# Kernel optimization log

Measured on AMD Instinct MI355X. Metric: run time of the kernel, lower is better.

The kernel has to match this reference:

```python
import jax, jax.numpy as jnp
import numpy as np

D = 64          # feature dim
H_POS = 64      # pos_mlp hidden
H_ATTN = 4 * D  # attn_mlp hidden
B, N = 1, 1024


def setup_inputs() -> dict:
    key = jax.random.key(0)
    ks = jax.random.split(key, 12)
    s = lambda fan_in: 1.0 / np.sqrt(fan_in)
    return {
        "x": jax.random.normal(ks[0], (B, N, D), jnp.float32),
        "pos": jax.random.normal(ks[1], (B, N, 2), jnp.float32),
        "Wq": jax.random.normal(ks[2], (D, D), jnp.float32) * s(D),
        "Wk": jax.random.normal(ks[3], (D, D), jnp.float32) * s(D),
        "Wv": jax.random.normal(ks[4], (D, D), jnp.float32) * s(D),
        "pW1": jax.random.normal(ks[5], (2, H_POS), jnp.float32) * s(2),
        "pb1": jnp.zeros((H_POS,), jnp.float32),
        "pW2": jax.random.normal(ks[6], (H_POS, D), jnp.float32) * s(H_POS),
        "pb2": jnp.zeros((D,), jnp.float32),
        "aW1": jax.random.normal(ks[7], (D, H_ATTN), jnp.float32) * s(D),
        "ab1": jnp.zeros((H_ATTN,), jnp.float32),
        "aW2": jax.random.normal(ks[8], (H_ATTN, D), jnp.float32) * s(H_ATTN),
        "ab2": jnp.zeros((D,), jnp.float32),
    }


def reference(x, pos, Wq, Wk, Wv, pW1, pb1, pW2, pb2, aW1, ab1, aW2, ab2):
    # projections: [b, n, d]
    q = x @ Wq
    k = x @ Wk
    v = x @ Wv
    # pairwise relative positions: [b, i, j, 2]
    rel_pos = pos[:, :, None, :] - pos[:, None, :, :]
    # pos MLP: [b, i, j, d]
    rpe = jax.nn.relu(rel_pos @ pW1 + pb1) @ pW2 + pb2
    # pairwise q - k: [b, i, j, d]
    qk_rel = q[:, :, None, :] - k[:, None, :, :]
    # values broadcast over i, plus positional embedding: [b, i, j, d]
    vv = v[:, None, :, :] + rpe
    # attention MLP on (qk_rel + rpe): [b, i, j, d]
    sim = jax.nn.relu((qk_rel + rpe) @ aW1 + ab1) @ aW2 + ab2
    # softmax over j (axis=-2), per-channel
    attn = jax.nn.softmax(sim, axis=-2)
    # weighted aggregation: [b, i, d]
    agg = jnp.einsum('bijd,bijd->bid', attn, vv)
    return agg
```

## Files before the change

### kernel.cpp

```cpp
#include <hip/hip_runtime.h>


typedef float f32x4 __attribute__((ext_vector_type(4)));
typedef int   i32x8 __attribute__((ext_vector_type(8)));
using sh8 = __attribute__((ext_vector_type(8))) short;

static constexpr int NPTS = 1024;

#if __has_builtin(__builtin_amdgcn_exp2f)
#define EXP2(x) __builtin_amdgcn_exp2f(x)
#else
#define EXP2(x) exp2f(x)
#endif

static constexpr size_t BEXT_OFF = 0;
static constexpr size_t AW2F_OFF = 65536;
static constexpr size_t PW2F_OFF = 98304;
static constexpr size_t CARR_OFF = 106496;
static constexpr size_t AI_OFF   = 107520;
static constexpr size_t QI_OFF   = 369664;
static constexpr size_t VPT_OFF  = 631808;
static constexpr size_t AJ_OFF   = 893952;
static constexpr size_t KN_OFF   = 1025024;

__device__ __forceinline__ unsigned short f2b_rne(float f) {
    unsigned u = __float_as_uint(f);
    u += 0x7fffu + ((u >> 16) & 1u);
    return (unsigned short)(u >> 16);
}
__device__ __forceinline__ unsigned pk2(float lo, float hi) {
    return __builtin_amdgcn_perm(__float_as_uint(hi), __float_as_uint(lo), 0x07060302);
}
__device__ __forceinline__ float b2f(unsigned short s) {
    return __uint_as_float(((unsigned)s) << 16);
}
__device__ __forceinline__ unsigned char f2fp8(float v) {
    return (unsigned char)(__builtin_amdgcn_cvt_pk_fp8_f32(v, 0.f, 0, false) & 0xff);
}
__device__ __forceinline__ unsigned pk4fp8(float a, float b, float c, float d) {
    int r = __builtin_amdgcn_cvt_pk_fp8_f32(a, b, 0, false);
    r = __builtin_amdgcn_cvt_pk_fp8_f32(c, d, r, true);
    return (unsigned)r;
}
__device__ __forceinline__ i32x8 ld32B(const void* p) {
    const uint4 a = ((const uint4*)p)[0];
    const uint4 b = ((const uint4*)p)[1];
    i32x8 r;
    r[0] = a.x; r[1] = a.y; r[2] = a.z; r[3] = a.w;
    r[4] = b.x; r[5] = b.y; r[6] = b.z; r[7] = b.w;
    return r;
}

__global__ void prep_all(const float* __restrict__ x, const float* __restrict__ pos,
                         const float* __restrict__ Wq, const float* __restrict__ Wk,
                         const float* __restrict__ Wv, const float* __restrict__ pW1,
                         const float* __restrict__ pb1, const float* __restrict__ pW2,
                         const float* __restrict__ pb2, const float* __restrict__ aW1,
                         const float* __restrict__ ab1, const float* __restrict__ aW2,
                         unsigned short* __restrict__ bextf, unsigned char* __restrict__ aw2f8,
                         unsigned short* __restrict__ pw2f, float* __restrict__ cArr,
                         float* __restrict__ qI, unsigned short* __restrict__ kN,
                         float* __restrict__ vPT, float* __restrict__ aI,
                         unsigned short* __restrict__ aJ)
{
    const int b = blockIdx.x;
    if (b < 209) {
        const int idx = b * 256 + threadIdx.x;
        if (idx < 32768) {
            const int k = idx >> 8, t = idx & 255;
            float val;
            if (k < 64) {
                float s = 0.f;
                for (int d = 0; d < 64; ++d) s = fmaf(pW2[k * 64 + d], aW1[d * 256 + t], s);
                val = s;
            } else {
                val = aW1[(k - 64) * 256 + t];
            }
            const int kc = k >> 5, kl = k & 31, qq = kl >> 3, e = kl & 7;
            const int ntg = t >> 4, tl = t & 15;
            bextf[(((size_t)(kc * 16 + ntg) * 64) + (qq * 16 + tl)) * 8 + e] = f2b_rne(val);
        } else if (idx < 49152) {
            const int r = idx - 32768;
            const int e = r & 31, lane = (r >> 5) & 63, wsl = (r >> 11) & 3, kb = r >> 13;
            const int q = lane >> 4, dl = lane & 15;
            const int kp = kb * 128 + q * 32 + e;
            const int t = 64 * (kp >> 6) + 16 * (kp & 3) + ((kp >> 2) & 15);
            const int d = 16 * wsl + dl;
            aw2f8[r] = f2fp8(aW2[t * 64 + d] * 1.4426950408889634f);
        } else if (idx < 53248) {
            const int r = idx - 49152;
            const int k = r >> 6, d = r & 63;
            const int kc = k >> 5, kl = k & 31, qq = kl >> 3, e = kl & 7;
            const int nt = d >> 4, dl = d & 15;
            pw2f[(((size_t)(kc * 4 + nt) * 64) + (qq * 16 + dl)) * 8 + e] = f2b_rne(pW2[k * 64 + d]);
        } else if (idx < 53504) {
            const int t = idx - 53248;
            float s = ab1[t];
            for (int d = 0; d < 64; ++d) s = fmaf(pb2[d], aW1[d * 256 + t], s);
            cArr[t] = s;
        }
    } else {
        const int t = threadIdx.x, sub = t >> 6, d = t & 63;
        const int i = (b - 209) * 4 + sub;
        __shared__ float xs[4][64];
        xs[sub][d] = x[i * 64 + d];
        __syncthreads();
        float q = 0.f, k = 0.f, v = 0.f;
        for (int e = 0; e < 64; ++e) {
            const float xe = xs[sub][e];
            q = fmaf(xe, Wq[e * 64 + d], q);
            k = fmaf(xe, Wk[e * 64 + d], k);
            v = fmaf(xe, Wv[e * 64 + d], v);
        }
        const float a = pos[i * 2] * pW1[d] + pos[i * 2 + 1] * pW1[64 + d];
        qI[i * 64 + d] = q;
        kN[i * 64 + d] = f2b_rne(-k);
        vPT[d * NPTS + i] = v + pb2[d];
        aI[i * 64 + d] = a + pb1[d];
        aJ[i * 64 + d] = f2b_rne(a);
    }
}

__global__ __launch_bounds__(256, 2) void ptl_main(
    const float* __restrict__ aI, const float* __restrict__ qI,
    const unsigned short* __restrict__ aJ, const unsigned short* __restrict__ kN,
    const float* __restrict__ vPT,
    const unsigned short* __restrict__ bextf, const unsigned char* __restrict__ aw2f8,
    const unsigned short* __restrict__ pw2f, const float* __restrict__ cArr,
    float* __restrict__ out)
{
    const int i    = blockIdx.x;
    const int tid  = threadIdx.x;
    const int w    = tid >> 6;
    const int lane = tid & 63;
    const int m    = lane & 15;
    const int q    = lane >> 4;

    __shared__ __align__(16) uint4 AfL[2][2][4][64];
    __shared__ __align__(16) unsigned char Hs[2][2][16 * 272];

    sh8 Bf[16];
#pragma unroll
    for (int kc = 0; kc < 4; ++kc)
#pragma unroll
        for (int nt = 0; nt < 4; ++nt)
            Bf[kc * 4 + nt] = *(const sh8*)(bextf + ((size_t)((kc * 16 + 4 * w + nt) * 64 + lane)) * 8);
    i32x8 W2f[2];
#pragma unroll
    for (int kb = 0; kb < 2; ++kb)
        W2f[kb] = ld32B(aw2f8 + ((size_t)((kb * 4 + w) * 64 + lane)) * 32);
    sh8 P2f[2];
#pragma unroll
    for (int kc = 0; kc < 2; ++kc)
        P2f[kc] = *(const sh8*)(pw2f + ((size_t)((kc * 4 + w) * 64 + lane)) * 8);

    float creg[4];
#pragma unroll
    for (int nt = 0; nt < 4; ++nt) creg[nt] = cArr[64 * w + 16 * nt + m];

    const int  half   = w & 1;
    const bool isRelu = (w < 2);
    const unsigned short* bsrc  = (isRelu ? aJ : kN) + m * 64 + half * 32 + q * 8;
    const float*          ibase = (isRelu ? aI : qI) + i * 64 + half * 32 + q * 8;
    float iv[8];
    *(float4*)(iv)     = *(const float4*)(ibase);
    *(float4*)(iv + 4) = *(const float4*)(ibase + 4);

#pragma unroll
    for (int s = 0; s < 2; ++s) {
        const sh8 raw = *(const sh8*)(bsrc + (size_t)(16 * s) * 64);
        float t[8];
#pragma unroll
        for (int e = 0; e < 8; ++e)
            t[e] = isRelu ? fmaxf(iv[e] - b2f((unsigned short)raw[e]), 0.f)
                          : iv[e] + b2f((unsigned short)raw[e]);
        uint4 pk;
        pk.x = pk2(t[0], t[1]); pk.y = pk2(t[2], t[3]);
        pk.z = pk2(t[4], t[5]); pk.w = pk2(t[6], t[7]);
        AfL[0][s][w][lane] = pk;
    }
    __syncthreads();

    float num = 0.f, den = 0.f;
    const f32x4 z4 = {0.f, 0.f, 0.f, 0.f};
    const float* vbase = vPT + (size_t)(16 * w + m) * NPTS;

    for (int n = 0; n < 32; ++n) {
        const int pb = n & 1, nb = pb ^ 1;
        const int j0 = n << 5;

        sh8 raw0, raw1;
        if (n < 31) {
            raw0 = *(const sh8*)(bsrc + (size_t)(j0 + 32) * 64);
            raw1 = *(const sh8*)(bsrc + (size_t)(j0 + 48) * 64);
        }
        const float4 vj0 = *(const float4*)(vbase + j0 + 4 * q);
        const float4 vj1 = *(const float4*)(vbase + j0 + 16 + 4 * q);

        const sh8 A00 = *(const sh8*)&AfL[pb][0][0][lane];
        const sh8 A01 = *(const sh8*)&AfL[pb][0][1][lane];
        const sh8 A02 = *(const sh8*)&AfL[pb][0][2][lane];
        const sh8 A03 = *(const sh8*)&AfL[pb][0][3][lane];
        {
            f32x4 acc[4];
#pragma unroll
            for (int nt = 0; nt < 4; ++nt) {
                const f32x4 cv = {creg[nt], creg[nt], creg[nt], creg[nt]};
                acc[nt] = __builtin_amdgcn_mfma_f32_16x16x32_bf16(A00, Bf[0 * 4 + nt], cv, 0, 0, 0);
                acc[nt] = __builtin_amdgcn_mfma_f32_16x16x32_bf16(A01, Bf[1 * 4 + nt], acc[nt], 0, 0, 0);
                acc[nt] = __builtin_amdgcn_mfma_f32_16x16x32_bf16(A02, Bf[2 * 4 + nt], acc[nt], 0, 0, 0);
                acc[nt] = __builtin_amdgcn_mfma_f32_16x16x32_bf16(A03, Bf[3 * 4 + nt], acc[nt], 0, 0, 0);
            }
            unsigned char* hw = Hs[pb][0] + (4 * q) * 272 + 64 * w + 4 * m;
#pragma unroll
            for (int r = 0; r < 4; ++r)
                *(unsigned*)(hw + r * 272) = pk4fp8(fmaxf(acc[0][r], 0.f), fmaxf(acc[1][r], 0.f),
                                                   fmaxf(acc[2][r], 0.f), fmaxf(acc[3][r], 0.f));
        }

        const sh8 A10 = *(const sh8*)&AfL[pb][1][0][lane];
        const sh8 A11 = *(const sh8*)&AfL[pb][1][1][lane];
        const sh8 A12 = *(const sh8*)&AfL[pb][1][2][lane];
        const sh8 A13 = *(const sh8*)&AfL[pb][1][3][lane];
        {
            f32x4 acc[4];
#pragma unroll
            for (int nt = 0; nt < 4; ++nt) {
                const f32x4 cv = {creg[nt], creg[nt], creg[nt], creg[nt]};
                acc[nt] = __builtin_amdgcn_mfma_f32_16x16x32_bf16(A10, Bf[0 * 4 + nt], cv, 0, 0, 0);
                acc[nt] = __builtin_amdgcn_mfma_f32_16x16x32_bf16(A11, Bf[1 * 4 + nt], acc[nt], 0, 0, 0);
                acc[nt] = __builtin_amdgcn_mfma_f32_16x16x32_bf16(A12, Bf[2 * 4 + nt], acc[nt], 0, 0, 0);
                acc[nt] = __builtin_amdgcn_mfma_f32_16x16x32_bf16(A13, Bf[3 * 4 + nt], acc[nt], 0, 0, 0);
            }
            unsigned char* hw = Hs[pb][1] + (4 * q) * 272 + 64 * w + 4 * m;
#pragma unroll
            for (int r = 0; r < 4; ++r)
                *(unsigned*)(hw + r * 272) = pk4fp8(fmaxf(acc[0][r], 0.f), fmaxf(acc[1][r], 0.f),
                                                   fmaxf(acc[2][r], 0.f), fmaxf(acc[3][r], 0.f));
        }

        const f32x4 vc0 = {vj0.x, vj0.y, vj0.z, vj0.w};
        const f32x4 vc1 = {vj1.x, vj1.y, vj1.z, vj1.w};
        f32x4 aR0 = __builtin_amdgcn_mfma_f32_16x16x32_bf16(A00, P2f[0], vc0, 0, 0, 0);
        aR0 = __builtin_amdgcn_mfma_f32_16x16x32_bf16(A01, P2f[1], aR0, 0, 0, 0);
        f32x4 aR1 = __builtin_amdgcn_mfma_f32_16x16x32_bf16(A10, P2f[0], vc1, 0, 0, 0);
        aR1 = __builtin_amdgcn_mfma_f32_16x16x32_bf16(A11, P2f[1], aR1, 0, 0, 0);

        if (n < 31) {
#pragma unroll
            for (int s = 0; s < 2; ++s) {
                const sh8 raw = s ? raw1 : raw0;
                float t[8];
#pragma unroll
                for (int e = 0; e < 8; ++e)
                    t[e] = isRelu ? fmaxf(iv[e] - b2f((unsigned short)raw[e]), 0.f)
                                  : iv[e] + b2f((unsigned short)raw[e]);
                uint4 pk;
                pk.x = pk2(t[0], t[1]); pk.y = pk2(t[2], t[3]);
                pk.z = pk2(t[4], t[5]); pk.w = pk2(t[6], t[7]);
                AfL[nb][s][w][lane] = pk;
            }
        }

        __syncthreads();

        f32x4 aS0 = z4, aS1 = z4;
#pragma unroll
        for (int kb = 0; kb < 2; ++kb) {
            const i32x8 h0 = ld32B(Hs[pb][0] + m * 272 + kb * 128 + 32 * q);
            aS0 = __builtin_amdgcn_mfma_scale_f32_16x16x128_f8f6f4(
                h0, W2f[kb], aS0, 0, 0, 0, 127, 0, 127);
            const i32x8 h1 = ld32B(Hs[pb][1] + m * 272 + kb * 128 + 32 * q);
            aS1 = __builtin_amdgcn_mfma_scale_f32_16x16x128_f8f6f4(
                h1, W2f[kb], aS1, 0, 0, 0, 127, 0, 127);
        }

#pragma unroll
        for (int r = 0; r < 4; ++r) {
            const float e0 = EXP2(aS0[r]);
            num = fmaf(e0, aR0[r], num);
            den += e0;
            const float e1 = EXP2(aS1[r]);
            num = fmaf(e1, aR1[r], num);
            den += e1;
        }
    }

    num += __shfl_xor(num, 16);
    num += __shfl_xor(num, 32);
    den += __shfl_xor(den, 16);
    den += __shfl_xor(den, 32);
    if (q == 0) out[i * 64 + 16 * w + m] = num / den;
}

extern "C" void kernel_launch(void* const* d_in, const int* in_sizes, int n_in,
                              void* d_out, int out_size, void* d_ws, size_t ws_size,
                              hipStream_t stream) {
    const float* x   = (const float*)d_in[0];
    const float* pos = (const float*)d_in[1];
    const float* Wq  = (const float*)d_in[2];
    const float* Wk  = (const float*)d_in[3];
    const float* Wv  = (const float*)d_in[4];
    const float* pW1 = (const float*)d_in[5];
    const float* pb1 = (const float*)d_in[6];
    const float* pW2 = (const float*)d_in[7];
    const float* pb2 = (const float*)d_in[8];
    const float* aW1 = (const float*)d_in[9];
    const float* ab1 = (const float*)d_in[10];
    const float* aW2 = (const float*)d_in[11];

    char* ws = (char*)d_ws;
    unsigned short* bextf = (unsigned short*)(ws + BEXT_OFF);
    unsigned char*  aw2f8 = (unsigned char*)(ws + AW2F_OFF);
    unsigned short* pw2f  = (unsigned short*)(ws + PW2F_OFF);
    float*          cArr  = (float*)(ws + CARR_OFF);
    float*          aIa   = (float*)(ws + AI_OFF);
    float*          qIa   = (float*)(ws + QI_OFF);
    float*          vPTa  = (float*)(ws + VPT_OFF);
    unsigned short* aJa   = (unsigned short*)(ws + AJ_OFF);
    unsigned short* kNa   = (unsigned short*)(ws + KN_OFF);

    prep_all<<<465, 256, 0, stream>>>(x, pos, Wq, Wk, Wv, pW1, pb1, pW2, pb2, aW1, ab1, aW2,
                                      bextf, aw2f8, pw2f, cArr, qIa, kNa, vPTa, aIa, aJa);
    ptl_main<<<NPTS, 256, 0, stream>>>(aIa, qIa, aJa, kNa, vPTa, bextf, aw2f8, pw2f, cArr,
                                       (float*)d_out);
}
```

Baseline: 183.2 us.

## Software-pipeline second-layer MLP and softmax accumulation by one iteration

```diff
diff --git a/kernel.cpp b/kernel.cpp
--- a/kernel.cpp
+++ b/kernel.cpp
@@ -183,6 +183,7 @@
 
     float num = 0.f, den = 0.f;
     const f32x4 z4 = {0.f, 0.f, 0.f, 0.f};
+    f32x4 aRp0 = z4, aRp1 = z4;
     const float* vbase = vPT + (size_t)(16 * w + m) * NPTS;
 
     for (int n = 0; n < 32; ++n) {
@@ -218,6 +219,14 @@
                                                    fmaxf(acc[2][r], 0.f), fmaxf(acc[3][r], 0.f));
         }
 
+        i32x8 h00, h01, h10, h11;
+        if (n) {
+            h00 = ld32B(Hs[nb][0] + m * 272 + 0   + 32 * q);
+            h01 = ld32B(Hs[nb][0] + m * 272 + 128 + 32 * q);
+            h10 = ld32B(Hs[nb][1] + m * 272 + 0   + 32 * q);
+            h11 = ld32B(Hs[nb][1] + m * 272 + 128 + 32 * q);
+        }
+
         const sh8 A10 = *(const sh8*)&AfL[pb][1][0][lane];
         const sh8 A11 = *(const sh8*)&AfL[pb][1][1][lane];
         const sh8 A12 = *(const sh8*)&AfL[pb][1][2][lane];
@@ -239,12 +248,35 @@
                                                    fmaxf(acc[2][r], 0.f), fmaxf(acc[3][r], 0.f));
         }
 
+        if (n) {
+            f32x4 aS0 = z4, aS1 = z4;
+            aS0 = __builtin_amdgcn_mfma_scale_f32_16x16x128_f8f6f4(
+                h00, W2f[0], aS0, 0, 0, 0, 127, 0, 127);
+            aS0 = __builtin_amdgcn_mfma_scale_f32_16x16x128_f8f6f4(
+                h01, W2f[1], aS0, 0, 0, 0, 127, 0, 127);
+            aS1 = __builtin_amdgcn_mfma_scale_f32_16x16x128_f8f6f4(
+                h10, W2f[0], aS1, 0, 0, 0, 127, 0, 127);
+            aS1 = __builtin_amdgcn_mfma_scale_f32_16x16x128_f8f6f4(
+                h11, W2f[1], aS1, 0, 0, 0, 127, 0, 127);
+#pragma unroll
+            for (int r = 0; r < 4; ++r) {
+                const float e0 = EXP2(aS0[r]);
+                num = fmaf(e0, aRp0[r], num);
+                den += e0;
+                const float e1 = EXP2(aS1[r]);
+                num = fmaf(e1, aRp1[r], num);
+                den += e1;
+            }
+        }
+
         const f32x4 vc0 = {vj0.x, vj0.y, vj0.z, vj0.w};
         const f32x4 vc1 = {vj1.x, vj1.y, vj1.z, vj1.w};
         f32x4 aR0 = __builtin_amdgcn_mfma_f32_16x16x32_bf16(A00, P2f[0], vc0, 0, 0, 0);
         aR0 = __builtin_amdgcn_mfma_f32_16x16x32_bf16(A01, P2f[1], aR0, 0, 0, 0);
         f32x4 aR1 = __builtin_amdgcn_mfma_f32_16x16x32_bf16(A10, P2f[0], vc1, 0, 0, 0);
         aR1 = __builtin_amdgcn_mfma_f32_16x16x32_bf16(A11, P2f[1], aR1, 0, 0, 0);
+        aRp0 = aR0;
+        aRp1 = aR1;
 
         if (n < 31) {
 #pragma unroll
@@ -263,25 +295,29 @@
         }
 
         __syncthreads();
-
+    }
+
+    {
         f32x4 aS0 = z4, aS1 = z4;
-#pragma unroll
-        for (int kb = 0; kb < 2; ++kb) {
-            const i32x8 h0 = ld32B(Hs[pb][0] + m * 272 + kb * 128 + 32 * q);
-            aS0 = __builtin_amdgcn_mfma_scale_f32_16x16x128_f8f6f4(
-                h0, W2f[kb], aS0, 0, 0, 0, 127, 0, 127);
-            const i32x8 h1 = ld32B(Hs[pb][1] + m * 272 + kb * 128 + 32 * q);
-            aS1 = __builtin_amdgcn_mfma_scale_f32_16x16x128_f8f6f4(
-                h1, W2f[kb], aS1, 0, 0, 0, 127, 0, 127);
-        }
-
+        const i32x8 h00 = ld32B(Hs[1][0] + m * 272 + 0   + 32 * q);
+        const i32x8 h01 = ld32B(Hs[1][0] + m * 272 + 128 + 32 * q);
+        const i32x8 h10 = ld32B(Hs[1][1] + m * 272 + 0   + 32 * q);
+        const i32x8 h11 = ld32B(Hs[1][1] + m * 272 + 128 + 32 * q);
+        aS0 = __builtin_amdgcn_mfma_scale_f32_16x16x128_f8f6f4(
+            h00, W2f[0], aS0, 0, 0, 0, 127, 0, 127);
+        aS0 = __builtin_amdgcn_mfma_scale_f32_16x16x128_f8f6f4(
+            h01, W2f[1], aS0, 0, 0, 0, 127, 0, 127);
+        aS1 = __builtin_amdgcn_mfma_scale_f32_16x16x128_f8f6f4(
+            h10, W2f[0], aS1, 0, 0, 0, 127, 0, 127);
+        aS1 = __builtin_amdgcn_mfma_scale_f32_16x16x128_f8f6f4(
+            h11, W2f[1], aS1, 0, 0, 0, 127, 0, 127);
 #pragma unroll
         for (int r = 0; r < 4; ++r) {
             const float e0 = EXP2(aS0[r]);
-            num = fmaf(e0, aR0[r], num);
+            num = fmaf(e0, aRp0[r], num);
             den += e0;
             const float e1 = EXP2(aS1[r]);
-            num = fmaf(e1, aR1[r], num);
+            num = fmaf(e1, aRp1[r], num);
             den += e1;
         }
     }
```

Result: no change. 180.8 us (-1.3%).

## Process two query points per block and software-pipeline the second attention GEMM

Applied to the files above, without the earlier changes.

```diff
diff --git a/kernel.cpp b/kernel.cpp
--- a/kernel.cpp
+++ b/kernel.cpp
@@ -129,15 +129,15 @@
     const unsigned short* __restrict__ pw2f, const float* __restrict__ cArr,
     float* __restrict__ out)
 {
-    const int i    = blockIdx.x;
+    const int i0   = blockIdx.x * 2;
     const int tid  = threadIdx.x;
     const int w    = tid >> 6;
     const int lane = tid & 63;
     const int m    = lane & 15;
     const int q    = lane >> 4;
 
-    __shared__ __align__(16) uint4 AfL[2][2][4][64];
-    __shared__ __align__(16) unsigned char Hs[2][2][16 * 272];
+    __shared__ __align__(16) uint4 AfL[2][2][2][4][64];
+    __shared__ __align__(16) unsigned char Hs[2][2][2][16 * 272];
 
     sh8 Bf[16];
 #pragma unroll
@@ -160,47 +160,38 @@
 
     const int  half   = w & 1;
     const bool isRelu = (w < 2);
-    const unsigned short* bsrc  = (isRelu ? aJ : kN) + m * 64 + half * 32 + q * 8;
-    const float*          ibase = (isRelu ? aI : qI) + i * 64 + half * 32 + q * 8;
-    float iv[8];
-    *(float4*)(iv)     = *(const float4*)(ibase);
-    *(float4*)(iv + 4) = *(const float4*)(ibase + 4);
-
-#pragma unroll
-    for (int s = 0; s < 2; ++s) {
-        const sh8 raw = *(const sh8*)(bsrc + (size_t)(16 * s) * 64);
-        float t[8];
-#pragma unroll
-        for (int e = 0; e < 8; ++e)
-            t[e] = isRelu ? fmaxf(iv[e] - b2f((unsigned short)raw[e]), 0.f)
-                          : iv[e] + b2f((unsigned short)raw[e]);
-        uint4 pk;
-        pk.x = pk2(t[0], t[1]); pk.y = pk2(t[2], t[3]);
-        pk.z = pk2(t[4], t[5]); pk.w = pk2(t[6], t[7]);
-        AfL[0][s][w][lane] = pk;
-    }
-    __syncthreads();
-
-    float num = 0.f, den = 0.f;
-    const f32x4 z4 = {0.f, 0.f, 0.f, 0.f};
-    const float* vbase = vPT + (size_t)(16 * w + m) * NPTS;
-
-    for (int n = 0; n < 32; ++n) {
-        const int pb = n & 1, nb = pb ^ 1;
-        const int j0 = n << 5;
-
-        sh8 raw0, raw1;
-        if (n < 31) {
-            raw0 = *(const sh8*)(bsrc + (size_t)(j0 + 32) * 64);
-            raw1 = *(const sh8*)(bsrc + (size_t)(j0 + 48) * 64);
-        }
-        const float4 vj0 = *(const float4*)(vbase + j0 + 4 * q);
-        const float4 vj1 = *(const float4*)(vbase + j0 + 16 + 4 * q);
-
-        const sh8 A00 = *(const sh8*)&AfL[pb][0][0][lane];
-        const sh8 A01 = *(const sh8*)&AfL[pb][0][1][lane];
-        const sh8 A02 = *(const sh8*)&AfL[pb][0][2][lane];
-        const sh8 A03 = *(const sh8*)&AfL[pb][0][3][lane];
+    const unsigned short* bsrc = (isRelu ? aJ : kN) + m * 64 + half * 32 + q * 8;
+    const float* ib0 = (isRelu ? aI : qI) + (size_t)i0 * 64 + half * 32 + q * 8;
+    const float* ib1 = ib0 + 64;
+    float iv0[8], iv1[8];
+    *(float4*)(iv0)     = *(const float4*)(ib0);
+    *(float4*)(iv0 + 4) = *(const float4*)(ib0 + 4);
+    *(float4*)(iv1)     = *(const float4*)(ib1);
+    *(float4*)(iv1 + 4) = *(const float4*)(ib1 + 4);
+
+    auto build2 = [&](int buf, int s, const sh8& raw) {
+        float t0[8], t1[8];
+#pragma unroll
+        for (int e = 0; e < 8; ++e) {
+            const float bj = b2f((unsigned short)raw[e]);
+            t0[e] = isRelu ? fmaxf(iv0[e] - bj, 0.f) : iv0[e] + bj;
+            t1[e] = isRelu ? fmaxf(iv1[e] - bj, 0.f) : iv1[e] + bj;
+        }
+        uint4 p0, p1;
+        p0.x = pk2(t0[0], t0[1]); p0.y = pk2(t0[2], t0[3]);
+        p0.z = pk2(t0[4], t0[5]); p0.w = pk2(t0[6], t0[7]);
+        p1.x = pk2(t1[0], t1[1]); p1.y = pk2(t1[2], t1[3]);
+        p1.z = pk2(t1[4], t1[5]); p1.w = pk2(t1[6], t1[7]);
+        AfL[buf][0][s][w][lane] = p0;
+        AfL[buf][1][s][w][lane] = p1;
+    };
+
+    auto g1g3 = [&](int buf, int qq, const f32x4& vc0, const f32x4& vc1,
+                    f32x4& aRn0, f32x4& aRn1) {
+        const sh8 A00 = *(const sh8*)&AfL[buf][qq][0][0][lane];
+        const sh8 A01 = *(const sh8*)&AfL[buf][qq][0][1][lane];
+        const sh8 A02 = *(const sh8*)&AfL[buf][qq][0][2][lane];
+        const sh8 A03 = *(const sh8*)&AfL[buf][qq][0][3][lane];
         {
             f32x4 acc[4];
 #pragma unroll
@@ -211,17 +202,16 @@
                 acc[nt] = __builtin_amdgcn_mfma_f32_16x16x32_bf16(A02, Bf[2 * 4 + nt], acc[nt], 0, 0, 0);
                 acc[nt] = __builtin_amdgcn_mfma_f32_16x16x32_bf16(A03, Bf[3 * 4 + nt], acc[nt], 0, 0, 0);
             }
-            unsigned char* hw = Hs[pb][0] + (4 * q) * 272 + 64 * w + 4 * m;
+            unsigned char* hw = Hs[buf][qq][0] + (4 * q) * 272 + 64 * w + 4 * m;
 #pragma unroll
             for (int r = 0; r < 4; ++r)
                 *(unsigned*)(hw + r * 272) = pk4fp8(fmaxf(acc[0][r], 0.f), fmaxf(acc[1][r], 0.f),
                                                    fmaxf(acc[2][r], 0.f), fmaxf(acc[3][r], 0.f));
         }
-
-        const sh8 A10 = *(const sh8*)&AfL[pb][1][0][lane];
-        const sh8 A11 = *(const sh8*)&AfL[pb][1][1][lane];
-        const sh8 A12 = *(const sh8*)&AfL[pb][1][2][lane];
-        const sh8 A13 = *(const sh8*)&AfL[pb][1][3][lane];
+        const sh8 A10 = *(const sh8*)&AfL[buf][qq][1][0][lane];
+        const sh8 A11 = *(const sh8*)&AfL[buf][qq][1][1][lane];
+        const sh8 A12 = *(const sh8*)&AfL[buf][qq][1][2][lane];
+        const sh8 A13 = *(const sh8*)&AfL[buf][qq][1][3][lane];
         {
             f32x4 acc[4];
 #pragma unroll
@@ -232,65 +222,102 @@
                 acc[nt] = __builtin_amdgcn_mfma_f32_16x16x32_bf16(A12, Bf[2 * 4 + nt], acc[nt], 0, 0, 0);
                 acc[nt] = __builtin_amdgcn_mfma_f32_16x16x32_bf16(A13, Bf[3 * 4 + nt], acc[nt], 0, 0, 0);
             }
-            unsigned char* hw = Hs[pb][1] + (4 * q) * 272 + 64 * w + 4 * m;
+            unsigned char* hw = Hs[buf][qq][1] + (4 * q) * 272 + 64 * w + 4 * m;
 #pragma unroll
             for (int r = 0; r < 4; ++r)
                 *(unsigned*)(hw + r * 272) = pk4fp8(fmaxf(acc[0][r], 0.f), fmaxf(acc[1][r], 0.f),
                                                    fmaxf(acc[2][r], 0.f), fmaxf(acc[3][r], 0.f));
         }
-
+        aRn0 = __builtin_amdgcn_mfma_f32_16x16x32_bf16(A00, P2f[0], vc0, 0, 0, 0);
+        aRn0 = __builtin_amdgcn_mfma_f32_16x16x32_bf16(A01, P2f[1], aRn0, 0, 0, 0);
+        aRn1 = __builtin_amdgcn_mfma_f32_16x16x32_bf16(A10, P2f[0], vc1, 0, 0, 0);
+        aRn1 = __builtin_amdgcn_mfma_f32_16x16x32_bf16(A11, P2f[1], aRn1, 0, 0, 0);
+    };
+
+    auto g2acc = [&](int buf, int qq, const f32x4& p0, const f32x4& p1,
+                     float& nm, float& dn) {
+        const f32x4 z4l = {0.f, 0.f, 0.f, 0.f};
+        const i32x8 h00 = ld32B(Hs[buf][qq][0] + m * 272 + 0   + 32 * q);
+        const i32x8 h01 = ld32B(Hs[buf][qq][0] + m * 272 + 128 + 32 * q);
+        const i32x8 h10 = ld32B(Hs[buf][qq][1] + m * 272 + 0   + 32 * q);
+        const i32x8 h11 = ld32B(Hs[buf][qq][1] + m * 272 + 128 + 32 * q);
+        f32x4 aS0 = z4l, aS1 = z4l;
+        aS0 = __builtin_amdgcn_mfma_scale_f32_16x16x128_f8f6f4(h00, W2f[0], aS0, 0, 0, 0, 127, 0, 127);
+        aS0 = __builtin_amdgcn_mfma_scale_f32_16x16x128_f8f6f4(h01, W2f[1], aS0, 0, 0, 0, 127, 0, 127);
+        aS1 = __builtin_amdgcn_mfma_scale_f32_16x16x128_f8f6f4(h10, W2f[0], aS1, 0, 0, 0, 127, 0, 127);
+        aS1 = __builtin_amdgcn_mfma_scale_f32_16x16x128_f8f6f4(h11, W2f[1], aS1, 0, 0, 0, 127, 0, 127);
+#pragma unroll
+        for (int r = 0; r < 4; ++r) {
+            const float e0 = EXP2(aS0[r]);
+            nm = fmaf(e0, p0[r], nm);
+            dn += e0;
+            const float e1 = EXP2(aS1[r]);
+            nm = fmaf(e1, p1[r], nm);
+            dn += e1;
+        }
+    };
+
+    {
+        const sh8 rA = *(const sh8*)(bsrc);
+        const sh8 rB = *(const sh8*)(bsrc + (size_t)16 * 64);
+        build2(0, 0, rA);
+        build2(0, 1, rB);
+    }
+    __syncthreads();
+
+    float num0 = 0.f, den0 = 0.f, num1 = 0.f, den1 = 0.f;
+    const f32x4 z4 = {0.f, 0.f, 0.f, 0.f};
+    f32x4 aRp00 = z4, aRp01 = z4, aRp10 = z4, aRp11 = z4;
+    const float* vbase = vPT + (size_t)(16 * w + m) * NPTS;
+
+    for (int n = 0; n < 32; ++n) {
+        const int pb = n & 1, nb = pb ^ 1;
+        const int j0 = n << 5;
+
+        sh8 raw0, raw1;
+        if (n < 31) {
+            raw0 = *(const sh8*)(bsrc + (size_t)(j0 + 32) * 64);
+            raw1 = *(const sh8*)(bsrc + (size_t)(j0 + 48) * 64);
+        }
+        const float4 vj0 = *(const float4*)(vbase + j0 + 4 * q);
+        const float4 vj1 = *(const float4*)(vbase + j0 + 16 + 4 * q);
         const f32x4 vc0 = {vj0.x, vj0.y, vj0.z, vj0.w};
         const f32x4 vc1 = {vj1.x, vj1.y, vj1.z, vj1.w};
-        f32x4 aR0 = __builtin_amdgcn_mfma_f32_16x16x32_bf16(A00, P2f[0], vc0, 0, 0, 0);
-        aR0 = __builtin_amdgcn_mfma_f32_16x16x32_bf16(A01, P2f[1], aR0, 0, 0, 0);
-        f32x4 aR1 = __builtin_amdgcn_mfma_f32_16x16x32_bf16(A10, P2f[0], vc1, 0, 0, 0);
-        aR1 = __builtin_amdgcn_mfma_f32_16x16x32_bf16(A11, P2f[1], aR1, 0, 0, 0);
+
+        f32x4 aRn00, aRn01, aRn10, aRn11;
+        g1g3(pb, 0, vc0, vc1, aRn00, aRn01);
+        g1g3(pb, 1, vc0, vc1, aRn10, aRn11);
+
+        if (n) {
+            g2acc(nb, 0, aRp00, aRp01, num0, den0);
+            g2acc(nb, 1, aRp10, aRp11, num1, den1);
+        }
+        aRp00 = aRn00; aRp01 = aRn01;
+        aRp10 = aRn10; aRp11 = aRn11;
 
         if (n < 31) {
-#pragma unroll
-            for (int s = 0; s < 2; ++s) {
-                const sh8 raw = s ? raw1 : raw0;
-                float t[8];
-#pragma unroll
-                for (int e = 0; e < 8; ++e)
-                    t[e] = isRelu ? fmaxf(iv[e] - b2f((unsigned short)raw[e]), 0.f)
-                                  : iv[e] + b2f((unsigned short)raw[e]);
-                uint4 pk;
-                pk.x = pk2(t[0], t[1]); pk.y = pk2(t[2], t[3]);
-                pk.z = pk2(t[4], t[5]); pk.w = pk2(t[6], t[7]);
-                AfL[nb][s][w][lane] = pk;
-            }
+            build2(nb, 0, raw0);
+            build2(nb, 1, raw1);
         }
 
         __syncthreads();
-
-        f32x4 aS0 = z4, aS1 = z4;
-#pragma unroll
-        for (int kb = 0; kb < 2; ++kb) {
-            const i32x8 h0 = ld32B(Hs[pb][0] + m * 272 + kb * 128 + 32 * q);
-            aS0 = __builtin_amdgcn_mfma_scale_f32_16x16x128_f8f6f4(
-                h0, W2f[kb], aS0, 0, 0, 0, 127, 0, 127);
-            const i32x8 h1 = ld32B(Hs[pb][1] + m * 272 + kb * 128 + 32 * q);
-            aS1 = __builtin_amdgcn_mfma_scale_f32_16x16x128_f8f6f4(
-                h1, W2f[kb], aS1, 0, 0, 0, 127, 0, 127);
-        }
-
-#pragma unroll
-        for (int r = 0; r < 4; ++r) {
-            const float e0 = EXP2(aS0[r]);
-            num = fmaf(e0, aR0[r], num);
-            den += e0;
-            const float e1 = EXP2(aS1[r]);
-            num = fmaf(e1, aR1[r], num);
-            den += e1;
-        }
     }
 
-    num += __shfl_xor(num, 16);
-    num += __shfl_xor(num, 32);
-    den += __shfl_xor(den, 16);
-    den += __shfl_xor(den, 32);
-    if (q == 0) out[i * 64 + 16 * w + m] = num / den;
+    g2acc(1, 0, aRp00, aRp01, num0, den0);
+    g2acc(1, 1, aRp10, aRp11, num1, den1);
+
+    num0 += __shfl_xor(num0, 16);
+    num0 += __shfl_xor(num0, 32);
+    den0 += __shfl_xor(den0, 16);
+    den0 += __shfl_xor(den0, 32);
+    num1 += __shfl_xor(num1, 16);
+    num1 += __shfl_xor(num1, 32);
+    den1 += __shfl_xor(den1, 16);
+    den1 += __shfl_xor(den1, 32);
+    if (q == 0) {
+        out[(size_t)i0 * 64 + 16 * w + m]       = num0 / den0;
+        out[(size_t)(i0 + 1) * 64 + 16 * w + m] = num1 / den1;
+    }
 }
 
 extern "C" void kernel_launch(void* const* d_in, const int* in_sizes, int n_in,
@@ -322,6 +349,6 @@
 
     prep_all<<<465, 256, 0, stream>>>(x, pos, Wq, Wk, Wv, pW1, pb1, pW2, pb2, aW1, ab1, aW2,
                                       bextf, aw2f8, pw2f, cArr, qIa, kNa, vPTa, aIa, aJa);
-    ptl_main<<<NPTS, 256, 0, stream>>>(aIa, qIa, aJa, kNa, vPTa, bextf, aw2f8, pw2f, cArr,
-                                       (float*)d_out);
-}
+    ptl_main<<<NPTS / 2, 256, 0, stream>>>(aIa, qIa, aJa, kNa, vPTa, bextf, aw2f8, pw2f, cArr,
+                                           (float*)d_out);
+}
```

Result: no change. 180.2 us (-1.7%).
